# Kernel tuning notes

Hardware: AMD Instinct MI355X
Metric: run time of the kernel (lower is better)

Reference implementation:

```python
import jax, jax.numpy as jnp
import numpy as np

N = 50000
E = 800000
IN_C, HID_C, OUT_C = 128, 128, 40
K = 3  # PyG TAGConv default number of hops


def setup_inputs() -> dict:
    key = jax.random.key(0)
    k1, k2, k3, k4, k5, k6, k7 = jax.random.split(key, 7)
    x = jax.random.normal(k1, (N, IN_C), dtype=jnp.float32)
    edge_index = jax.random.randint(k2, (2, E), 0, N, dtype=jnp.int64)
    # Linear((K+1)*in, out) weights (stored as [in_total, out] for x @ W)
    s1 = 1.0 / np.sqrt((K + 1) * IN_C)
    s2 = 1.0 / np.sqrt((K + 1) * HID_C)
    W1 = jax.random.uniform(k3, ((K + 1) * IN_C, HID_C), jnp.float32, -s1, s1)
    b1 = jax.random.uniform(k4, (HID_C,), jnp.float32, -s1, s1)
    W2 = jax.random.uniform(k5, ((K + 1) * HID_C, OUT_C), jnp.float32, -s2, s2)
    b2 = jax.random.uniform(k6, (OUT_C,), jnp.float32, -s2, s2)
    return {"x": x, "edge_index": edge_index, "W1": W1, "b1": b1, "W2": W2, "b2": b2}


def _sym_norm(src, dst):
    # GCN-style symmetric normalization: deg computed on destination (col)
    deg = jax.ops.segment_sum(jnp.ones((E,), jnp.float32), dst, num_segments=N)
    dis = jnp.where(deg > 0, jax.lax.rsqrt(jnp.maximum(deg, 1.0)), 0.0)
    return dis[src] * dis[dst]  # [E]


def _tag_layer(x, src, dst, norm, W, b):
    xs = [x]
    h = x
    for _ in range(K):
        h = jax.ops.segment_sum(h[src] * norm[:, None], dst, num_segments=N)
        xs.append(h)
    return jnp.concatenate(xs, axis=1) @ W + b


def reference(x, edge_index, W1, b1, W2, b2):
    src, dst = edge_index[0], edge_index[1]
    norm = _sym_norm(src, dst)
    h = jax.nn.relu(_tag_layer(x, src, dst, norm, W1, b1))
    # F.dropout(training=False) is identity at inference
    h = _tag_layer(h, src, dst, norm, W2, b2)
    return jax.nn.log_softmax(h, axis=1)
```

## Files before the change

kernel.cpp:

```cpp
#include <hip/hip_runtime.h>
#include <hip/hip_bf16.h>

#define NNODES 50000
#define NROWP  50176
#define NEDGES 800000
#define KHOP 3
#define SCAN_NB 49
#define NBKT 196
#define BCAP 6144
#define ABLK 400
#define ACH  2000

typedef __attribute__((ext_vector_type(8))) short short8v;
typedef __attribute__((ext_vector_type(8))) __bf16 bf16x8;
typedef __attribute__((ext_vector_type(4))) float f32x4;

__device__ inline unsigned short f2bf(float f) {
  unsigned u = __builtin_bit_cast(unsigned, f);
  u += 0x7fffu + ((u >> 16) & 1u);
  return (unsigned short)(u >> 16);
}
__device__ inline float bf2f(unsigned short h) {
  return __builtin_bit_cast(float, (unsigned)h << 16);
}
__device__ inline float bflo(unsigned u) { return __builtin_bit_cast(float, u << 16); }
__device__ inline float bfhi(unsigned u) { return __builtin_bit_cast(float, u & 0xffff0000u); }

__device__ inline void gload_lds16(const void* g, void* l) {
  __builtin_amdgcn_global_load_lds(
      (const __attribute__((address_space(1))) unsigned int*)g,
      (__attribute__((address_space(3))) unsigned int*)l, 16, 0, 0);
}

__device__ inline f32x4 mfma_bf16(bf16x8 a, bf16x8 b, f32x4 c) {
  return __builtin_amdgcn_mfma_f32_16x16x32_bf16(a, b, c, 0, 0, 0);
}

__global__ __launch_bounds__(256) void bucketA_kernel(
    const int* __restrict__ src, const int* __restrict__ dst,
    int* __restrict__ bcur, int2* __restrict__ bkt) {
  __shared__ int2 eb[ACH];
  __shared__ int hist[256];
  __shared__ int base[256];
  int tid = threadIdx.x;
  int e0 = blockIdx.x * ACH;
  int cnt = NEDGES - e0; if (cnt > ACH) cnt = ACH;
  hist[tid] = 0;
  __syncthreads();
  for (int i = tid; i < cnt; i += 256) {
    int s = src[e0 + i], d = dst[e0 + i];
    eb[i] = make_int2(s, d);
    atomicAdd(&hist[d >> 8], 1);
  }
  __syncthreads();
  base[tid] = atomicAdd(&bcur[tid], hist[tid]);
  hist[tid] = 0;
  __syncthreads();
  for (int i = tid; i < cnt; i += 256) {
    int2 e = eb[i];
    int b = e.y >> 8;
    int off = atomicAdd(&hist[b], 1);
    bkt[(size_t)b * BCAP + base[b] + off] = e;
  }
}

__global__ __launch_bounds__(256) void histB_kernel(
    const int* __restrict__ bcur, const int2* __restrict__ bkt,
    int* __restrict__ cnt, int n) {
  __shared__ int h[256];
  int b = blockIdx.x, tid = threadIdx.x;
  h[tid] = 0;
  __syncthreads();
  int sz = bcur[b];
  for (int i = tid; i < sz; i += 256)
    atomicAdd(&h[bkt[(size_t)b * BCAP + i].y & 255], 1);
  __syncthreads();
  int node = b * 256 + tid;
  if (node < n) cnt[node] = h[tid];
}

__global__ __launch_bounds__(256) void bsum_kernel(const int* __restrict__ cnt,
                                                   int* __restrict__ bsums, int n) {
  __shared__ int sd[256];
  int tid = threadIdx.x;
  int base = blockIdx.x * 1024 + tid * 4;
  int s = 0;
  if (base + 4 <= n) {
    int4 v = *(const int4*)&cnt[base];
    s = v.x + v.y + v.z + v.w;
  }
  sd[tid] = s;
  __syncthreads();
  for (int o = 128; o; o >>= 1) {
    if (tid < o) sd[tid] += sd[tid + o];
    __syncthreads();
  }
  if (tid == 0) bsums[blockIdx.x] = sd[0];
}

__global__ __launch_bounds__(64) void bscan_kernel(const int* __restrict__ bsums,
                                                   int* __restrict__ boff,
                                                   int* __restrict__ row_ptr,
                                                   int nb, int n) {
  int tid = threadIdx.x;
  int own = (tid < nb) ? bsums[tid] : 0;
  int v = own;
#pragma unroll
  for (int o = 1; o < 64; o <<= 1) {
    int t = __shfl_up(v, o, 64);
    if (tid >= o) v += t;
  }
  if (tid < nb) boff[tid] = v - own;
  if (tid == 63) row_ptr[n] = v;
}

__global__ __launch_bounds__(256) void bfinal_kernel(const int* __restrict__ cnt,
                                                     const int* __restrict__ boff,
                                                     int* __restrict__ row_ptr,
                                                     float* __restrict__ dis, int n) {
  __shared__ int sd[256];
  int tid = threadIdx.x;
  int base = blockIdx.x * 1024 + tid * 4;
  int4 v = make_int4(0, 0, 0, 0);
  bool ok = (base + 4 <= n);
  if (ok) v = *(const int4*)&cnt[base];
  int s = v.x + v.y + v.z + v.w;
  sd[tid] = s;
  __syncthreads();
  for (int o = 1; o < 256; o <<= 1) {
    int t = (tid >= o) ? sd[tid - o] : 0;
    __syncthreads();
    sd[tid] += t;
    __syncthreads();
  }
  if (ok) {
    int run = boff[blockIdx.x] + sd[tid] - s;
    int4 rp;
    rp.x = run;
    rp.y = run + v.x;
    rp.z = rp.y + v.y;
    rp.w = rp.z + v.z;
    *(int4*)&row_ptr[base] = rp;
    float4 dv;
    dv.x = (v.x > 0) ? rsqrtf((float)v.x) : 0.f;
    dv.y = (v.y > 0) ? rsqrtf((float)v.y) : 0.f;
    dv.z = (v.z > 0) ? rsqrtf((float)v.z) : 0.f;
    dv.w = (v.w > 0) ? rsqrtf((float)v.w) : 0.f;
    *(float4*)&dis[base] = dv;
  }
}

__global__ __launch_bounds__(256) void scatB_kernel(
    const int* __restrict__ bcur, const int2* __restrict__ bkt,
    const int* __restrict__ row_ptr, const float* __restrict__ dis,
    int2* __restrict__ csr, int n) {
  __shared__ int cur[256];
  int b = blockIdx.x, tid = threadIdx.x;
  int node = b * 256 + tid;
  cur[tid] = (node < n) ? row_ptr[node] : 0;
  __syncthreads();
  int sz = bcur[b];
  for (int i = tid; i < sz; i += 256) {
    int2 e = bkt[(size_t)b * BCAP + i];
    int pos = atomicAdd(&cur[e.y & 255], 1);
    int2 ent;
    ent.x = e.x;
    ent.y = __float_as_int(dis[e.x] * dis[e.y]);
    csr[pos] = ent;
  }
}

__global__ void wprep_kernel(const float* __restrict__ W1, const float* __restrict__ W2,
                             unsigned short* __restrict__ W1t,
                             unsigned short* __restrict__ W2pt) {
  int t = blockIdx.x * blockDim.x + threadIdx.x;
  if (t < 512 * 128) {
    int c = t >> 9, k = t & 511;
    W1t[t] = f2bf(W1[(size_t)k * 128 + c]);
  } else if (t < 512 * 128 + 160 * 128) {
    int u = t - 512 * 128;
    int q = u >> 7, r = u & 127;
    int k = q / 40, c = q - k * 40;
    W2pt[u] = f2bf(W2[(size_t)(k * 128 + r) * 40 + c]);
  }
}

__global__ void copyx_kernel(const float* __restrict__ x, unsigned short* __restrict__ P, int n) {
  int t = blockIdx.x * blockDim.x + threadIdx.x;
  int i = t >> 5;
  int c4 = (t & 31) << 2;
  if (i < n) {
    float4 v = *(const float4*)&x[(size_t)i * 128 + c4];
    unsigned lo = (unsigned)f2bf(v.x) | ((unsigned)f2bf(v.y) << 16);
    unsigned hi = (unsigned)f2bf(v.z) | ((unsigned)f2bf(v.w) << 16);
    uint2 o; o.x = lo; o.y = hi;
    *(uint2*)&P[(size_t)i * 512 + c4] = o;
  }
}

__global__ __launch_bounds__(256) void prop128b_kernel(
    const unsigned short* __restrict__ in, unsigned short* __restrict__ out,
    const int* __restrict__ row_ptr, const int2* __restrict__ csr, int n) {
  int node = (int)((blockIdx.x * blockDim.x + threadIdx.x) >> 6);
  int lane = threadIdx.x & 63;
  if (node >= n) return;
  int beg = row_ptr[node], end = row_ptr[node + 1];
  int deg = end - beg;
  int2 ent = make_int2(0, 0);
  if (lane < deg) ent = csr[beg + lane];
  float ax = 0.f, ay = 0.f;
  int m = deg < 64 ? deg : 64;
  int j = 0;
  for (; j + 4 <= m; j += 4) {
    int s0 = __shfl(ent.x, j, 64);
    int s1 = __shfl(ent.x, j + 1, 64);
    int s2 = __shfl(ent.x, j + 2, 64);
    int s3 = __shfl(ent.x, j + 3, 64);
    float w0 = __int_as_float(__shfl(ent.y, j, 64));
    float w1 = __int_as_float(__shfl(ent.y, j + 1, 64));
    float w2 = __int_as_float(__shfl(ent.y, j + 2, 64));
    float w3 = __int_as_float(__shfl(ent.y, j + 3, 64));
    unsigned p0 = *(const unsigned*)&in[(size_t)s0 * 512 + 2 * lane];
    unsigned p1 = *(const unsigned*)&in[(size_t)s1 * 512 + 2 * lane];
    unsigned p2 = *(const unsigned*)&in[(size_t)s2 * 512 + 2 * lane];
    unsigned p3 = *(const unsigned*)&in[(size_t)s3 * 512 + 2 * lane];
    ax = fmaf(w0, bflo(p0), ax); ay = fmaf(w0, bfhi(p0), ay);
    ax = fmaf(w1, bflo(p1), ax); ay = fmaf(w1, bfhi(p1), ay);
    ax = fmaf(w2, bflo(p2), ax); ay = fmaf(w2, bfhi(p2), ay);
    ax = fmaf(w3, bflo(p3), ax); ay = fmaf(w3, bfhi(p3), ay);
  }
  for (; j < m; ++j) {
    int s0 = __shfl(ent.x, j, 64);
    float w0 = __int_as_float(__shfl(ent.y, j, 64));
    unsigned p0 = *(const unsigned*)&in[(size_t)s0 * 512 + 2 * lane];
    ax = fmaf(w0, bflo(p0), ax); ay = fmaf(w0, bfhi(p0), ay);
  }
  for (int t = beg + 64; t < end; ++t) {
    int2 e0 = csr[t];
    float w0 = __int_as_float(e0.y);
    unsigned p0 = *(const unsigned*)&in[(size_t)e0.x * 512 + 2 * lane];
    ax = fmaf(w0, bflo(p0), ax); ay = fmaf(w0, bfhi(p0), ay);
  }
  unsigned o = (unsigned)f2bf(ax) | ((unsigned)f2bf(ay) << 16);
  *(unsigned*)&out[(size_t)node * 512 + 2 * lane] = o;
}

__global__ __launch_bounds__(256) void gemm1m_kernel(
    const unsigned short* __restrict__ A,
    const unsigned short* __restrict__ Bt,
    const float* __restrict__ bias,
    unsigned short* __restrict__ H) {
  __shared__ short As[64 * 32];
  __shared__ short Bs[128 * 32];
  const int tid = threadIdx.x;
  const int lane = tid & 63;
  const int w = tid >> 6;
  const int wr = w & 1;
  const int wc = w >> 1;
  const int row0 = blockIdx.x * 64;
  f32x4 acc[2][4];
#pragma unroll
  for (int i = 0; i < 2; ++i)
#pragma unroll
    for (int j = 0; j < 4; ++j) acc[i][j] = (f32x4)0.f;

  const int lrow = lane >> 2;
  const int lkp = lane & 3;

  for (int k0 = 0; k0 < 512; k0 += 32) {
    gload_lds16(A + (size_t)(row0 + w * 16 + lrow) * 512 + k0 + lkp * 8, &As[w * 512]);
    gload_lds16(Bt + (size_t)(w * 16 + lrow) * 512 + k0 + lkp * 8, &Bs[w * 512]);
    gload_lds16(Bt + (size_t)((w + 4) * 16 + lrow) * 512 + k0 + lkp * 8, &Bs[(w + 4) * 512]);
    __syncthreads();
    const int kg = lane >> 4, rr = lane & 15;
    bf16x8 af[2], bfr[4];
#pragma unroll
    for (int mr = 0; mr < 2; ++mr)
      af[mr] = __builtin_bit_cast(bf16x8,
          *(const short8v*)&As[(wr * 32 + mr * 16 + rr) * 32 + kg * 8]);
#pragma unroll
    for (int nr = 0; nr < 4; ++nr)
      bfr[nr] = __builtin_bit_cast(bf16x8,
          *(const short8v*)&Bs[(wc * 64 + nr * 16 + rr) * 32 + kg * 8]);
#pragma unroll
    for (int mr = 0; mr < 2; ++mr)
#pragma unroll
      for (int nr = 0; nr < 4; ++nr)
        acc[mr][nr] = mfma_bf16(af[mr], bfr[nr], acc[mr][nr]);
    __syncthreads();
  }
  const int cg = lane >> 4, cl = lane & 15;
#pragma unroll
  for (int mr = 0; mr < 2; ++mr)
#pragma unroll
    for (int nr = 0; nr < 4; ++nr) {
      int col = wc * 64 + nr * 16 + cl;
      float bv = bias[col];
#pragma unroll
      for (int j = 0; j < 4; ++j) {
        int row = row0 + wr * 32 + mr * 16 + cg * 4 + j;
        H[(size_t)row * 128 + col] = f2bf(fmaxf(acc[mr][nr][j] + bv, 0.f));
      }
    }
}

__global__ __launch_bounds__(256) void gemm2m_kernel(
    const unsigned short* __restrict__ A,
    const unsigned short* __restrict__ Bt,
    unsigned short* __restrict__ G) {
  __shared__ short As[64 * 32];
  __shared__ short Bs[160 * 32];
  const int tid = threadIdx.x;
  const int lane = tid & 63;
  const int w = tid >> 6;
  const int row0 = blockIdx.x * 64;
  f32x4 acc[10];
#pragma unroll
  for (int i = 0; i < 10; ++i) acc[i] = (f32x4)0.f;
  const int lrow = lane >> 2, lkp = lane & 3;

  for (int k0 = 0; k0 < 128; k0 += 32) {
    gload_lds16(A + (size_t)(row0 + w * 16 + lrow) * 128 + k0 + lkp * 8, &As[w * 512]);
    for (int c = w; c < 10; c += 4)
      gload_lds16(Bt + (size_t)(c * 16 + lrow) * 128 + k0 + lkp * 8, &Bs[c * 512]);
    __syncthreads();
    const int kg = lane >> 4, rr = lane & 15;
    bf16x8 af = __builtin_bit_cast(bf16x8,
        *(const short8v*)&As[(w * 16 + rr) * 32 + kg * 8]);
#pragma unroll
    for (int nr = 0; nr < 10; ++nr) {
      bf16x8 bfr = __builtin_bit_cast(bf16x8,
          *(const short8v*)&Bs[(nr * 16 + rr) * 32 + kg * 8]);
      acc[nr] = mfma_bf16(af, bfr, acc[nr]);
    }
    __syncthreads();
  }
  const int cg = lane >> 4, cl = lane & 15;
#pragma unroll
  for (int nr = 0; nr < 10; ++nr) {
    int col = nr * 16 + cl;
    int k = col / 40;
    int o = col - k * 40;
#pragma unroll
    for (int j = 0; j < 4; ++j) {
      int row = row0 + w * 16 + cg * 4 + j;
      G[(size_t)k * NROWP * 40 + (size_t)row * 40 + o] = f2bf(acc[nr][j]);
    }
  }
}

__global__ __launch_bounds__(256) void prop40b_kernel(
    const unsigned short* __restrict__ in,
    const unsigned short* __restrict__ add,
    unsigned short* __restrict__ out,
    const int* __restrict__ row_ptr, const int2* __restrict__ csr, int n) {
  int node = (int)((blockIdx.x * blockDim.x + threadIdx.x) >> 6);
  int lane = threadIdx.x & 63;
  if (node >= n) return;
  int beg = row_ptr[node], end = row_ptr[node + 1];
  int deg = end - beg;
  int2 ent = make_int2(0, 0);
  if (lane < deg) ent = csr[beg + lane];
  float acc = (lane < 40) ? bf2f(add[(size_t)node * 40 + lane]) : 0.f;
  int m = deg < 64 ? deg : 64;
  int j = 0;
  for (; j + 4 <= m; j += 4) {
    int s0 = __shfl(ent.x, j, 64);
    int s1 = __shfl(ent.x, j + 1, 64);
    int s2 = __shfl(ent.x, j + 2, 64);
    int s3 = __shfl(ent.x, j + 3, 64);
    float w0 = __int_as_float(__shfl(ent.y, j, 64));
    float w1 = __int_as_float(__shfl(ent.y, j + 1, 64));
    float w2 = __int_as_float(__shfl(ent.y, j + 2, 64));
    float w3 = __int_as_float(__shfl(ent.y, j + 3, 64));
    if (lane < 40) {
      float v0 = bf2f(in[(size_t)s0 * 40 + lane]);
      float v1 = bf2f(in[(size_t)s1 * 40 + lane]);
      float v2 = bf2f(in[(size_t)s2 * 40 + lane]);
      float v3 = bf2f(in[(size_t)s3 * 40 + lane]);
      acc = fmaf(w0, v0, acc);
      acc = fmaf(w1, v1, acc);
      acc = fmaf(w2, v2, acc);
      acc = fmaf(w3, v3, acc);
    }
  }
  for (; j < m; ++j) {
    int s0 = __shfl(ent.x, j, 64);
    float w0 = __int_as_float(__shfl(ent.y, j, 64));
    if (lane < 40) acc = fmaf(w0, bf2f(in[(size_t)s0 * 40 + lane]), acc);
  }
  for (int t = beg + 64; t < end; ++t) {
    int2 e0 = csr[t];
    if (lane < 40)
      acc = fmaf(__int_as_float(e0.y), bf2f(in[(size_t)e0.x * 40 + lane]), acc);
  }
  if (lane < 40) out[(size_t)node * 40 + lane] = f2bf(acc);
}

__global__ __launch_bounds__(256) void prop40b_lsm_kernel(
    const unsigned short* __restrict__ in,
    const unsigned short* __restrict__ add,
    const float* __restrict__ b2,
    float* __restrict__ out,
    const int* __restrict__ row_ptr, const int2* __restrict__ csr, int n) {
  int node = (int)((blockIdx.x * blockDim.x + threadIdx.x) >> 6);
  int lane = threadIdx.x & 63;
  if (node >= n) return;
  int beg = row_ptr[node], end = row_ptr[node + 1];
  int deg = end - beg;
  int2 ent = make_int2(0, 0);
  if (lane < deg) ent = csr[beg + lane];
  float acc = (lane < 40) ? bf2f(add[(size_t)node * 40 + lane]) : 0.f;
  int m = deg < 64 ? deg : 64;
  int j = 0;
  for (; j + 4 <= m; j += 4) {
    int s0 = __shfl(ent.x, j, 64);
    int s1 = __shfl(ent.x, j + 1, 64);
    int s2 = __shfl(ent.x, j + 2, 64);
    int s3 = __shfl(ent.x, j + 3, 64);
    float w0 = __int_as_float(__shfl(ent.y, j, 64));
    float w1 = __int_as_float(__shfl(ent.y, j + 1, 64));
    float w2 = __int_as_float(__shfl(ent.y, j + 2, 64));
    float w3 = __int_as_float(__shfl(ent.y, j + 3, 64));
    if (lane < 40) {
      float v0 = bf2f(in[(size_t)s0 * 40 + lane]);
      float v1 = bf2f(in[(size_t)s1 * 40 + lane]);
      float v2 = bf2f(in[(size_t)s2 * 40 + lane]);
      float v3 = bf2f(in[(size_t)s3 * 40 + lane]);
      acc = fmaf(w0, v0, acc);
      acc = fmaf(w1, v1, acc);
      acc = fmaf(w2, v2, acc);
      acc = fmaf(w3, v3, acc);
    }
  }
  for (; j < m; ++j) {
    int s0 = __shfl(ent.x, j, 64);
    float w0 = __int_as_float(__shfl(ent.y, j, 64));
    if (lane < 40) acc = fmaf(w0, bf2f(in[(size_t)s0 * 40 + lane]), acc);
  }
  for (int t = beg + 64; t < end; ++t) {
    int2 e0 = csr[t];
    if (lane < 40)
      acc = fmaf(__int_as_float(e0.y), bf2f(in[(size_t)e0.x * 40 + lane]), acc);
  }
  float v = (lane < 40) ? acc + b2[lane] : -__builtin_inff();
  float mx = v;
#pragma unroll
  for (int o = 32; o; o >>= 1) mx = fmaxf(mx, __shfl_xor(mx, o, 64));
  float p = (lane < 40) ? expf(v - mx) : 0.f;
  float s = p;
#pragma unroll
  for (int o = 32; o; o >>= 1) s += __shfl_xor(s, o, 64);
  if (lane < 40) out[(size_t)node * 40 + lane] = v - mx - logf(s);
}

extern "C" void kernel_launch(void* const* d_in, const int* in_sizes, int n_in,
                              void* d_out, int out_size, void* d_ws, size_t ws_size,
                              hipStream_t stream) {
  const float* x  = (const float*)d_in[0];
  const int*   ei = (const int*)d_in[1];
  const float* W1 = (const float*)d_in[2];
  const float* b1 = (const float*)d_in[3];
  const float* W2 = (const float*)d_in[4];
  const float* b2 = (const float*)d_in[5];
  const int* srcv = ei;
  const int* dstv = ei + NEDGES;
  float* out = (float*)d_out;

  char* wsb = (char*)d_ws;
  size_t off = 0;
  auto alloc = [&](size_t bytes) {
    char* p = wsb + off;
    off += (bytes + 255) & ~(size_t)255;
    return p;
  };
  int*            cnt     = (int*)            alloc((size_t)NNODES * 4);
  float*          dis     = (float*)          alloc((size_t)NNODES * 4);
  int*            row_ptr = (int*)            alloc(((size_t)NNODES + 1) * 4);
  int*            bcur    = (int*)            alloc((size_t)256 * 4);
  int*            bsums   = (int*)            alloc((size_t)SCAN_NB * 4);
  int*            boff    = (int*)            alloc((size_t)SCAN_NB * 4);
  int2*           bkt     = (int2*)           alloc((size_t)NBKT * BCAP * 8);
  int2*           csr     = (int2*)           alloc((size_t)NEDGES * 8);
  unsigned short* W1t     = (unsigned short*) alloc((size_t)128 * 512 * 2);
  unsigned short* W2pt    = (unsigned short*) alloc((size_t)160 * 128 * 2);
  unsigned short* P       = (unsigned short*) alloc((size_t)NROWP * 512 * 2);
  unsigned short* H       = (unsigned short*) alloc((size_t)NROWP * 128 * 2);
  unsigned short* G       = (unsigned short*) alloc((size_t)4 * NROWP * 40 * 2);
  unsigned short* tb      = (unsigned short*) alloc((size_t)NNODES * 40 * 2);
  unsigned short* t2      = (unsigned short*) alloc((size_t)NNODES * 40 * 2);

  unsigned short* G0 = G;
  unsigned short* G1 = G + (size_t)1 * NROWP * 40;
  unsigned short* G2 = G + (size_t)2 * NROWP * 40;
  unsigned short* G3 = G + (size_t)3 * NROWP * 40;

  hipMemsetAsync(bcur, 0, 256 * 4, stream);
  bucketA_kernel<<<ABLK, 256, 0, stream>>>(srcv, dstv, bcur, bkt);
  histB_kernel<<<NBKT, 256, 0, stream>>>(bcur, bkt, cnt, NNODES);
  bsum_kernel<<<SCAN_NB, 256, 0, stream>>>(cnt, bsums, NNODES);
  bscan_kernel<<<1, 64, 0, stream>>>(bsums, boff, row_ptr, SCAN_NB, NNODES);
  bfinal_kernel<<<SCAN_NB, 256, 0, stream>>>(cnt, boff, row_ptr, dis, NNODES);
  scatB_kernel<<<NBKT, 256, 0, stream>>>(bcur, bkt, row_ptr, dis, csr, NNODES);
  wprep_kernel<<<(512 * 128 + 160 * 128 + 255) / 256, 256, 0, stream>>>(W1, W2, W1t, W2pt);
  copyx_kernel<<<((NNODES * 32) + 255) / 256, 256, 0, stream>>>(x, P, NNODES);

  const int prop_blocks = (NNODES * 64 + 255) / 256;
  for (int k = 1; k <= KHOP; ++k)
    prop128b_kernel<<<prop_blocks, 256, 0, stream>>>(P + 128 * (k - 1), P + 128 * k,
                                                     row_ptr, csr, NNODES);
  const int gemm_blocks = (NNODES + 63) / 64;
  gemm1m_kernel<<<gemm_blocks, 256, 0, stream>>>(P, W1t, b1, H);
  gemm2m_kernel<<<gemm_blocks, 256, 0, stream>>>(H, W2pt, G);
  prop40b_kernel<<<prop_blocks, 256, 0, stream>>>(G3, G2, tb, row_ptr, csr, NNODES);
  prop40b_kernel<<<prop_blocks, 256, 0, stream>>>(tb, G1, t2, row_ptr, csr, NNODES);
  prop40b_lsm_kernel<<<prop_blocks, 256, 0, stream>>>(t2, G0, b2, out, row_ptr, csr, NNODES);
}
```

Measured before the change: 259.6 us.

## Split wavefront into 4 edge groups with wide vector gathers in propagation

The propagation kernels now split each 64-lane wavefront into four 16-lane groups. Each group gathers a different neighbour row with 16-byte loads for the 128-wide features, or 8-byte loads for the 40-wide ones, and the four partial sums are combined with cross-lane shuffles at the end. To allow aligned vector loads, the 40-column intermediate buffers (G, tb, t2) are padded to a 64-element row stride. This is meant to cut the number of load instructions per edge and keep more edges in flight per wavefront. The cost is an extra shuffle reduction, wasted lanes on padding columns, and extra bytes moved for the padded rows.

```diff
diff --git a/kernel.cpp b/kernel.cpp
--- a/kernel.cpp
+++ b/kernel.cpp
@@ -34,6 +34,25 @@
 
 __device__ inline f32x4 mfma_bf16(bf16x8 a, bf16x8 b, f32x4 c) {
   return __builtin_amdgcn_mfma_f32_16x16x32_bf16(a, b, c, 0, 0, 0);
+}
+
+__device__ inline void fma8(float* acc, float w, short8v v) {
+  uint4 u = __builtin_bit_cast(uint4, v);
+  acc[0] = fmaf(w, bflo(u.x), acc[0]);
+  acc[1] = fmaf(w, bfhi(u.x), acc[1]);
+  acc[2] = fmaf(w, bflo(u.y), acc[2]);
+  acc[3] = fmaf(w, bfhi(u.y), acc[3]);
+  acc[4] = fmaf(w, bflo(u.z), acc[4]);
+  acc[5] = fmaf(w, bfhi(u.z), acc[5]);
+  acc[6] = fmaf(w, bflo(u.w), acc[6]);
+  acc[7] = fmaf(w, bfhi(u.w), acc[7]);
+}
+
+__device__ inline void fma4(float* acc, float w, uint2 v) {
+  acc[0] = fmaf(w, bflo(v.x), acc[0]);
+  acc[1] = fmaf(w, bfhi(v.x), acc[1]);
+  acc[2] = fmaf(w, bflo(v.y), acc[2]);
+  acc[3] = fmaf(w, bfhi(v.y), acc[3]);
 }
 
 __global__ __launch_bounds__(256) void bucketA_kernel(
@@ -198,7 +217,7 @@
   }
 }
 
-__global__ __launch_bounds__(256) void prop128b_kernel(
+__global__ __launch_bounds__(256) void prop128c_kernel(
     const unsigned short* __restrict__ in, unsigned short* __restrict__ out,
     const int* __restrict__ row_ptr, const int2* __restrict__ csr, int n) {
   int node = (int)((blockIdx.x * blockDim.x + threadIdx.x) >> 6);
@@ -208,41 +227,38 @@
   int deg = end - beg;
   int2 ent = make_int2(0, 0);
   if (lane < deg) ent = csr[beg + lane];
-  float ax = 0.f, ay = 0.f;
+  const int grp = lane >> 4, sub = lane & 15;
+  float acc[8] = {0.f, 0.f, 0.f, 0.f, 0.f, 0.f, 0.f, 0.f};
   int m = deg < 64 ? deg : 64;
-  int j = 0;
-  for (; j + 4 <= m; j += 4) {
-    int s0 = __shfl(ent.x, j, 64);
-    int s1 = __shfl(ent.x, j + 1, 64);
-    int s2 = __shfl(ent.x, j + 2, 64);
-    int s3 = __shfl(ent.x, j + 3, 64);
-    float w0 = __int_as_float(__shfl(ent.y, j, 64));
-    float w1 = __int_as_float(__shfl(ent.y, j + 1, 64));
-    float w2 = __int_as_float(__shfl(ent.y, j + 2, 64));
-    float w3 = __int_as_float(__shfl(ent.y, j + 3, 64));
-    unsigned p0 = *(const unsigned*)&in[(size_t)s0 * 512 + 2 * lane];
-    unsigned p1 = *(const unsigned*)&in[(size_t)s1 * 512 + 2 * lane];
-    unsigned p2 = *(const unsigned*)&in[(size_t)s2 * 512 + 2 * lane];
-    unsigned p3 = *(const unsigned*)&in[(size_t)s3 * 512 + 2 * lane];
-    ax = fmaf(w0, bflo(p0), ax); ay = fmaf(w0, bfhi(p0), ay);
-    ax = fmaf(w1, bflo(p1), ax); ay = fmaf(w1, bfhi(p1), ay);
-    ax = fmaf(w2, bflo(p2), ax); ay = fmaf(w2, bfhi(p2), ay);
-    ax = fmaf(w3, bflo(p3), ax); ay = fmaf(w3, bfhi(p3), ay);
-  }
-  for (; j < m; ++j) {
-    int s0 = __shfl(ent.x, j, 64);
-    float w0 = __int_as_float(__shfl(ent.y, j, 64));
-    unsigned p0 = *(const unsigned*)&in[(size_t)s0 * 512 + 2 * lane];
-    ax = fmaf(w0, bflo(p0), ax); ay = fmaf(w0, bfhi(p0), ay);
+  for (int j = 0; j < m; j += 4) {
+    int idx = j + grp;
+    bool act = idx < m;
+    int ic = act ? idx : m - 1;
+    int s = __shfl(ent.x, ic, 64);
+    float w = __int_as_float(__shfl(ent.y, ic, 64));
+    if (!act) w = 0.f;
+    short8v v = *(const short8v*)(in + (size_t)s * 512 + sub * 8);
+    fma8(acc, w, v);
   }
   for (int t = beg + 64; t < end; ++t) {
     int2 e0 = csr[t];
-    float w0 = __int_as_float(e0.y);
-    unsigned p0 = *(const unsigned*)&in[(size_t)e0.x * 512 + 2 * lane];
-    ax = fmaf(w0, bflo(p0), ax); ay = fmaf(w0, bfhi(p0), ay);
-  }
-  unsigned o = (unsigned)f2bf(ax) | ((unsigned)f2bf(ay) << 16);
-  *(unsigned*)&out[(size_t)node * 512 + 2 * lane] = o;
+    float w = (grp == 0) ? __int_as_float(e0.y) : 0.f;
+    short8v v = *(const short8v*)(in + (size_t)e0.x * 512 + sub * 8);
+    fma8(acc, w, v);
+  }
+#pragma unroll
+  for (int i = 0; i < 8; ++i) {
+    acc[i] += __shfl_xor(acc[i], 16, 64);
+    acc[i] += __shfl_xor(acc[i], 32, 64);
+  }
+  if (grp == 0) {
+    uint4 r;
+    r.x = (unsigned)f2bf(acc[0]) | ((unsigned)f2bf(acc[1]) << 16);
+    r.y = (unsigned)f2bf(acc[2]) | ((unsigned)f2bf(acc[3]) << 16);
+    r.z = (unsigned)f2bf(acc[4]) | ((unsigned)f2bf(acc[5]) << 16);
+    r.w = (unsigned)f2bf(acc[6]) | ((unsigned)f2bf(acc[7]) << 16);
+    *(uint4*)(out + (size_t)node * 512 + sub * 8) = r;
+  }
 }
 
 __global__ __launch_bounds__(256) void gemm1m_kernel(
@@ -344,12 +360,12 @@
 #pragma unroll
     for (int j = 0; j < 4; ++j) {
       int row = row0 + w * 16 + cg * 4 + j;
-      G[(size_t)k * NROWP * 40 + (size_t)row * 40 + o] = f2bf(acc[nr][j]);
+      G[(size_t)k * NROWP * 64 + (size_t)row * 64 + o] = f2bf(acc[nr][j]);
     }
   }
 }
 
-__global__ __launch_bounds__(256) void prop40b_kernel(
+__global__ __launch_bounds__(256) void prop40c_kernel(
     const unsigned short* __restrict__ in,
     const unsigned short* __restrict__ add,
     unsigned short* __restrict__ out,
@@ -361,43 +377,44 @@
   int deg = end - beg;
   int2 ent = make_int2(0, 0);
   if (lane < deg) ent = csr[beg + lane];
-  float acc = (lane < 40) ? bf2f(add[(size_t)node * 40 + lane]) : 0.f;
+  const int grp = lane >> 4, sub = lane & 15;
+  float acc[4] = {0.f, 0.f, 0.f, 0.f};
+  if (grp == 0) {
+    uint2 a = *(const uint2*)(add + (size_t)node * 64 + sub * 4);
+    acc[0] = bflo(a.x); acc[1] = bfhi(a.x);
+    acc[2] = bflo(a.y); acc[3] = bfhi(a.y);
+  }
   int m = deg < 64 ? deg : 64;
-  int j = 0;
-  for (; j + 4 <= m; j += 4) {
-    int s0 = __shfl(ent.x, j, 64);
-    int s1 = __shfl(ent.x, j + 1, 64);
-    int s2 = __shfl(ent.x, j + 2, 64);
-    int s3 = __shfl(ent.x, j + 3, 64);
-    float w0 = __int_as_float(__shfl(ent.y, j, 64));
-    float w1 = __int_as_float(__shfl(ent.y, j + 1, 64));
-    float w2 = __int_as_float(__shfl(ent.y, j + 2, 64));
-    float w3 = __int_as_float(__shfl(ent.y, j + 3, 64));
-    if (lane < 40) {
-      float v0 = bf2f(in[(size_t)s0 * 40 + lane]);
-      float v1 = bf2f(in[(size_t)s1 * 40 + lane]);
-      float v2 = bf2f(in[(size_t)s2 * 40 + lane]);
-      float v3 = bf2f(in[(size_t)s3 * 40 + lane]);
-      acc = fmaf(w0, v0, acc);
-      acc = fmaf(w1, v1, acc);
-      acc = fmaf(w2, v2, acc);
-      acc = fmaf(w3, v3, acc);
-    }
-  }
-  for (; j < m; ++j) {
-    int s0 = __shfl(ent.x, j, 64);
-    float w0 = __int_as_float(__shfl(ent.y, j, 64));
-    if (lane < 40) acc = fmaf(w0, bf2f(in[(size_t)s0 * 40 + lane]), acc);
+  for (int j = 0; j < m; j += 4) {
+    int idx = j + grp;
+    bool act = idx < m;
+    int ic = act ? idx : m - 1;
+    int s = __shfl(ent.x, ic, 64);
+    float w = __int_as_float(__shfl(ent.y, ic, 64));
+    if (!act) w = 0.f;
+    uint2 v = *(const uint2*)(in + (size_t)s * 64 + sub * 4);
+    fma4(acc, w, v);
   }
   for (int t = beg + 64; t < end; ++t) {
     int2 e0 = csr[t];
-    if (lane < 40)
-      acc = fmaf(__int_as_float(e0.y), bf2f(in[(size_t)e0.x * 40 + lane]), acc);
-  }
-  if (lane < 40) out[(size_t)node * 40 + lane] = f2bf(acc);
-}
-
-__global__ __launch_bounds__(256) void prop40b_lsm_kernel(
+    float w = (grp == 0) ? __int_as_float(e0.y) : 0.f;
+    uint2 v = *(const uint2*)(in + (size_t)e0.x * 64 + sub * 4);
+    fma4(acc, w, v);
+  }
+#pragma unroll
+  for (int i = 0; i < 4; ++i) {
+    acc[i] += __shfl_xor(acc[i], 16, 64);
+    acc[i] += __shfl_xor(acc[i], 32, 64);
+  }
+  if (grp == 0) {
+    uint2 r;
+    r.x = (unsigned)f2bf(acc[0]) | ((unsigned)f2bf(acc[1]) << 16);
+    r.y = (unsigned)f2bf(acc[2]) | ((unsigned)f2bf(acc[3]) << 16);
+    *(uint2*)(out + (size_t)node * 64 + sub * 4) = r;
+  }
+}
+
+__global__ __launch_bounds__(256) void prop40c_lsm_kernel(
     const unsigned short* __restrict__ in,
     const unsigned short* __restrict__ add,
     const float* __restrict__ b2,
@@ -410,48 +427,59 @@
   int deg = end - beg;
   int2 ent = make_int2(0, 0);
   if (lane < deg) ent = csr[beg + lane];
-  float acc = (lane < 40) ? bf2f(add[(size_t)node * 40 + lane]) : 0.f;
+  const int grp = lane >> 4, sub = lane & 15;
+  float acc[4] = {0.f, 0.f, 0.f, 0.f};
+  if (grp == 0) {
+    uint2 a = *(const uint2*)(add + (size_t)node * 64 + sub * 4);
+    acc[0] = bflo(a.x); acc[1] = bfhi(a.x);
+    acc[2] = bflo(a.y); acc[3] = bfhi(a.y);
+  }
   int m = deg < 64 ? deg : 64;
-  int j = 0;
-  for (; j + 4 <= m; j += 4) {
-    int s0 = __shfl(ent.x, j, 64);
-    int s1 = __shfl(ent.x, j + 1, 64);
-    int s2 = __shfl(ent.x, j + 2, 64);
-    int s3 = __shfl(ent.x, j + 3, 64);
-    float w0 = __int_as_float(__shfl(ent.y, j, 64));
-    float w1 = __int_as_float(__shfl(ent.y, j + 1, 64));
-    float w2 = __int_as_float(__shfl(ent.y, j + 2, 64));
-    float w3 = __int_as_float(__shfl(ent.y, j + 3, 64));
-    if (lane < 40) {
-      float v0 = bf2f(in[(size_t)s0 * 40 + lane]);
-      float v1 = bf2f(in[(size_t)s1 * 40 + lane]);
-      float v2 = bf2f(in[(size_t)s2 * 40 + lane]);
-      float v3 = bf2f(in[(size_t)s3 * 40 + lane]);
-      acc = fmaf(w0, v0, acc);
-      acc = fmaf(w1, v1, acc);
-      acc = fmaf(w2, v2, acc);
-      acc = fmaf(w3, v3, acc);
-    }
-  }
-  for (; j < m; ++j) {
-    int s0 = __shfl(ent.x, j, 64);
-    float w0 = __int_as_float(__shfl(ent.y, j, 64));
-    if (lane < 40) acc = fmaf(w0, bf2f(in[(size_t)s0 * 40 + lane]), acc);
+  for (int j = 0; j < m; j += 4) {
+    int idx = j + grp;
+    bool act = idx < m;
+    int ic = act ? idx : m - 1;
+    int s = __shfl(ent.x, ic, 64);
+    float w = __int_as_float(__shfl(ent.y, ic, 64));
+    if (!act) w = 0.f;
+    uint2 v = *(const uint2*)(in + (size_t)s * 64 + sub * 4);
+    fma4(acc, w, v);
   }
   for (int t = beg + 64; t < end; ++t) {
     int2 e0 = csr[t];
-    if (lane < 40)
-      acc = fmaf(__int_as_float(e0.y), bf2f(in[(size_t)e0.x * 40 + lane]), acc);
-  }
-  float v = (lane < 40) ? acc + b2[lane] : -__builtin_inff();
-  float mx = v;
-#pragma unroll
-  for (int o = 32; o; o >>= 1) mx = fmaxf(mx, __shfl_xor(mx, o, 64));
-  float p = (lane < 40) ? expf(v - mx) : 0.f;
-  float s = p;
-#pragma unroll
-  for (int o = 32; o; o >>= 1) s += __shfl_xor(s, o, 64);
-  if (lane < 40) out[(size_t)node * 40 + lane] = v - mx - logf(s);
+    float w = (grp == 0) ? __int_as_float(e0.y) : 0.f;
+    uint2 v = *(const uint2*)(in + (size_t)e0.x * 64 + sub * 4);
+    fma4(acc, w, v);
+  }
+#pragma unroll
+  for (int i = 0; i < 4; ++i) {
+    acc[i] += __shfl_xor(acc[i], 16, 64);
+    acc[i] += __shfl_xor(acc[i], 32, 64);
+  }
+  bool val = (sub < 10);
+  float vv[4];
+  if (val) {
+    float4 bv = *(const float4*)(b2 + sub * 4);
+    vv[0] = acc[0] + bv.x; vv[1] = acc[1] + bv.y;
+    vv[2] = acc[2] + bv.z; vv[3] = acc[3] + bv.w;
+  } else {
+    vv[0] = vv[1] = vv[2] = vv[3] = -__builtin_inff();
+  }
+  float mx = fmaxf(fmaxf(vv[0], vv[1]), fmaxf(vv[2], vv[3]));
+#pragma unroll
+  for (int o = 1; o < 16; o <<= 1) mx = fmaxf(mx, __shfl_xor(mx, o, 64));
+  float s = 0.f;
+  if (val)
+    s = expf(vv[0] - mx) + expf(vv[1] - mx) + expf(vv[2] - mx) + expf(vv[3] - mx);
+#pragma unroll
+  for (int o = 1; o < 16; o <<= 1) s += __shfl_xor(s, o, 64);
+  if (val) {
+    float ls = logf(s);
+    float4 o4;
+    o4.x = vv[0] - mx - ls; o4.y = vv[1] - mx - ls;
+    o4.z = vv[2] - mx - ls; o4.w = vv[3] - mx - ls;
+    *(float4*)(out + (size_t)node * 40 + sub * 4) = o4;
+  }
 }
 
 extern "C" void kernel_launch(void* const* d_in, const int* in_sizes, int n_in,
@@ -486,14 +514,14 @@
   unsigned short* W2pt    = (unsigned short*) alloc((size_t)160 * 128 * 2);
   unsigned short* P       = (unsigned short*) alloc((size_t)NROWP * 512 * 2);
   unsigned short* H       = (unsigned short*) alloc((size_t)NROWP * 128 * 2);
-  unsigned short* G       = (unsigned short*) alloc((size_t)4 * NROWP * 40 * 2);
-  unsigned short* tb      = (unsigned short*) alloc((size_t)NNODES * 40 * 2);
-  unsigned short* t2      = (unsigned short*) alloc((size_t)NNODES * 40 * 2);
+  unsigned short* G       = (unsigned short*) alloc((size_t)4 * NROWP * 64 * 2);
+  unsigned short* tb      = (unsigned short*) alloc((size_t)NNODES * 64 * 2);
+  unsigned short* t2      = (unsigned short*) alloc((size_t)NNODES * 64 * 2);
 
   unsigned short* G0 = G;
-  unsigned short* G1 = G + (size_t)1 * NROWP * 40;
-  unsigned short* G2 = G + (size_t)2 * NROWP * 40;
-  unsigned short* G3 = G + (size_t)3 * NROWP * 40;
+  unsigned short* G1 = G + (size_t)1 * NROWP * 64;
+  unsigned short* G2 = G + (size_t)2 * NROWP * 64;
+  unsigned short* G3 = G + (size_t)3 * NROWP * 64;
 
   hipMemsetAsync(bcur, 0, 256 * 4, stream);
   bucketA_kernel<<<ABLK, 256, 0, stream>>>(srcv, dstv, bcur, bkt);
@@ -507,12 +535,12 @@
 
   const int prop_blocks = (NNODES * 64 + 255) / 256;
   for (int k = 1; k <= KHOP; ++k)
-    prop128b_kernel<<<prop_blocks, 256, 0, stream>>>(P + 128 * (k - 1), P + 128 * k,
+    prop128c_kernel<<<prop_blocks, 256, 0, stream>>>(P + 128 * (k - 1), P + 128 * k,
                                                      row_ptr, csr, NNODES);
   const int gemm_blocks = (NNODES + 63) / 64;
   gemm1m_kernel<<<gemm_blocks, 256, 0, stream>>>(P, W1t, b1, H);
   gemm2m_kernel<<<gemm_blocks, 256, 0, stream>>>(H, W2pt, G);
-  prop40b_kernel<<<prop_blocks, 256, 0, stream>>>(G3, G2, tb, row_ptr, csr, NNODES);
-  prop40b_kernel<<<prop_blocks, 256, 0, stream>>>(tb, G1, t2, row_ptr, csr, NNODES);
-  prop40b_lsm_kernel<<<prop_blocks, 256, 0, stream>>>(t2, G0, b2, out, row_ptr, csr, NNODES);
-}
+  prop40c_kernel<<<prop_blocks, 256, 0, stream>>>(G3, G2, tb, row_ptr, csr, NNODES);
+  prop40c_kernel<<<prop_blocks, 256, 0, stream>>>(tb, G1, t2, row_ptr, csr, NNODES);
+  prop40c_lsm_kernel<<<prop_blocks, 256, 0, stream>>>(t2, G0, b2, out, row_ptr, csr, NNODES);
+}
```

After: 254.3 us. 2.0% less time.
